# Performance work log

Hardware: AMD Instinct MI355X
Metric: run time of the kernel (lower is better)

The kernel has to match this reference:

```python
import jax, jax.numpy as jnp
import numpy as np

N, L, H, D = 2, 4096, 12, 64
HD = H * D

def setup_inputs() -> dict:
    key = jax.random.key(0)
    ks = jax.random.split(key, 5)
    s = 1.0 / np.sqrt(HD)  # keep projections well-scaled
    return {
        "x": jax.random.normal(ks[0], (N, L, HD), dtype=jnp.float32),
        "Wq": jax.random.normal(ks[1], (HD, HD), dtype=jnp.float32) * s,
        "bq": jnp.zeros((HD,), dtype=jnp.float32),
        "Wk": jax.random.normal(ks[2], (HD, HD), dtype=jnp.float32) * s,
        "bk": jnp.zeros((HD,), dtype=jnp.float32),
        "Wv": jax.random.normal(ks[3], (HD, HD), dtype=jnp.float32) * s,
        "bv": jnp.zeros((HD,), dtype=jnp.float32),
        "Wo": jax.random.normal(ks[4], (HD, HD), dtype=jnp.float32) * s,
        "bo": jnp.zeros((HD,), dtype=jnp.float32),
        "train": 0,
    }

def reference(x, Wq, bq, Wk, bk, Wv, bv, Wo, bo, train):
    n, l, hd = x.shape
    h, d = H, D
    # QKV projections (hk.Linear: x @ W + b), reshape to (n, l, h, d)
    q = (x @ Wq + bq).reshape(n, l, h, d)
    k = (x @ Wk + bk).reshape(n, l, h, d)
    v = (x @ Wv + bv).reshape(n, l, h, d)
    # scores: (n, q, k, h), scaled by sqrt(key_size)
    qkt = jnp.einsum('nqhd,nkhd->nqkh', q, k) / jnp.sqrt(jnp.float32(d))
    attn = jax.nn.softmax(qkt, axis=2)
    # eval mode: dropout_rate is 0.0, so dropout is identity
    o = jnp.einsum('nqkh,nkhd->nqhd', attn, v).reshape(n, l, hd)
    return o @ Wo + bo
```

## Files before the change

### kernel.cpp

```cpp
#include <hip/hip_runtime.h>

#define NN 2
#define LL 4096
#define HH 12
#define DD 64
#define HD_ 768
#define M_TOT (NN * LL)
#define KVSTRIDE 262144

typedef __bf16 bf16_t;
typedef _Float16 f16_t;
typedef __bf16 bf16x8 __attribute__((ext_vector_type(8)));
typedef __bf16 bf16x4 __attribute__((ext_vector_type(4)));
typedef _Float16 f16x2 __attribute__((ext_vector_type(2)));
typedef _Float16 f16x4 __attribute__((ext_vector_type(4)));
typedef _Float16 f16x8 __attribute__((ext_vector_type(8)));
typedef float floatx4 __attribute__((ext_vector_type(4)));
typedef float floatx16 __attribute__((ext_vector_type(16)));

#define QSCALE 0.1803368801111f

__device__ __forceinline__ void async_load16(const void* g, void* l) {
    __builtin_amdgcn_global_load_lds(
        (const __attribute__((address_space(1))) unsigned int*)(g),
        (__attribute__((address_space(3))) unsigned int*)(l),
        16, 0, 0);
}

__device__ __forceinline__ f16x2 pkrtz(float a, float b) {
    return __builtin_bit_cast(f16x2, __builtin_amdgcn_cvt_pkrtz(a, b));
}

__global__ void cvt_kernel(const float* __restrict__ src, bf16_t* __restrict__ dst, int n4) {
    int i = blockIdx.x * blockDim.x + threadIdx.x;
    if (i < n4) {
        const float4 v = ((const float4*)src)[i];
        bf16_t* d = dst + (size_t)i * 4;
        d[0] = (bf16_t)v.x; d[1] = (bf16_t)v.y; d[2] = (bf16_t)v.z; d[3] = (bf16_t)v.w;
    }
}

struct WtArgs { const float* W[4]; bf16_t* Wt[4]; };
__global__ __launch_bounds__(256) void cvt_wt_kernel(WtArgs a) {
    __shared__ bf16_t T[64 * 65];
    const int z = blockIdx.z;
    const int k0 = blockIdx.y * 64, n0 = blockIdx.x * 64;
    const int tid = threadIdx.x;
    {
        const int k = tid >> 2;
        const int nc = (tid & 3) * 16;
        const float* src = a.W[z] + (size_t)(k0 + k) * HD_ + n0 + nc;
        for (int i = 0; i < 4; ++i) {
            float4 v = *(const float4*)(src + i * 4);
            T[(nc + i * 4 + 0) * 65 + k] = (bf16_t)v.x;
            T[(nc + i * 4 + 1) * 65 + k] = (bf16_t)v.y;
            T[(nc + i * 4 + 2) * 65 + k] = (bf16_t)v.z;
            T[(nc + i * 4 + 3) * 65 + k] = (bf16_t)v.w;
        }
    }
    __syncthreads();
    {
        const int n = tid >> 2;
        const int kc = (tid & 3) * 16;
        bf16_t* dst = a.Wt[z] + (size_t)(n0 + n) * HD_ + k0 + kc;
        bf16x8 v0, v1;
        for (int j = 0; j < 8; ++j) { v0[j] = T[n * 65 + kc + j]; v1[j] = T[n * 65 + kc + 8 + j]; }
        *(bf16x8*)dst = v0;
        *(bf16x8*)(dst + 8) = v1;
    }
}

__device__ __forceinline__ void gemm_tile128(
    const bf16_t* __restrict__ A, const bf16_t* __restrict__ Bt,
    bf16_t* As, bf16_t* Bs, int m0, int n0, floatx4 (&acc)[4][4])
{
    const int tid  = threadIdx.x;
    const int w    = tid >> 6, lane = tid & 63;
    const int quad = lane >> 4, l16 = lane & 15;
    const int wm = w >> 1, wn = w & 1;
    const int rsub = lane >> 3;
    const int csub = (lane & 7) * 8;

    const bf16_t* aBase = A + (size_t)(m0 + w * 32 + rsub) * HD_ + csub;
    const bf16_t* bBase = Bt + (size_t)(n0 + w * 32 + rsub) * HD_ + csub;

    for (int kt = 0; kt < HD_; kt += 64) {
        __syncthreads();
        for (int i = 0; i < 4; ++i) {
            const int ar = w * 32 + i * 8;
            async_load16(aBase + (size_t)i * 8 * HD_ + kt, As + ar * 64 + lane * 8);
            async_load16(bBase + (size_t)i * 8 * HD_ + kt, Bs + ar * 64 + lane * 8);
        }
        __syncthreads();
        for (int ks = 0; ks < 2; ++ks) {
            bf16x8 af[4], bf[4];
            for (int mi = 0; mi < 4; ++mi)
                af[mi] = *(const bf16x8*)&As[(wm * 64 + mi * 16 + l16) * 64 + ks * 32 + quad * 8];
            for (int ni = 0; ni < 4; ++ni)
                bf[ni] = *(const bf16x8*)&Bs[(wn * 64 + ni * 16 + l16) * 64 + ks * 32 + quad * 8];
            for (int mi = 0; mi < 4; ++mi)
                for (int ni = 0; ni < 4; ++ni)
                    acc[mi][ni] = __builtin_amdgcn_mfma_f32_16x16x32_bf16(
                        af[mi], bf[ni], acc[mi][ni], 0, 0, 0);
        }
    }
}

struct QKVArgs {
    const bf16_t* Bt[3];
    const float* bias[3];
    void* out[3];
};
__global__ __launch_bounds__(256) void gemm_qkv_kernel(const bf16_t* __restrict__ A, QKVArgs p)
{
    __shared__ __align__(16) bf16_t S[2 * 128 * 64];
    const int z = blockIdx.z;
    const int m0 = blockIdx.y * 128, n0 = blockIdx.x * 128;

    floatx4 acc[4][4] = {};
    gemm_tile128(A, p.Bt[z], S, S + 8192, m0, n0, acc);

    const int tid  = threadIdx.x;
    const int lane = tid & 63;
    const int quad = lane >> 4, l16 = lane & 15;
    const int w    = tid >> 6;
    const int wm = w >> 1, wn = w & 1;
    const float scale = (z == 0) ? QSCALE : 1.0f;
    const float* bias = p.bias[z];

    __syncthreads();
    for (int ni = 0; ni < 4; ++ni) {
        const int dl = ni * 16 + l16;
        const float bv = bias[n0 + wn * 64 + dl];
        for (int mi = 0; mi < 4; ++mi) {
            for (int r = 0; r < 4; ++r) {
                const int ll = wm * 64 + mi * 16 + quad * 4 + r;
                const float val = (acc[mi][ni][r] + bv) * scale;
                int off;
                if (z == 0)
                    off = ll * 64 + dl;
                else if (z == 1)
                    off = ((ll >> 5) * 4 + (dl >> 4)) * 512
                        + ((ll & 31) + 32 * ((dl >> 3) & 1)) * 8 + (dl & 7);
                else
                    off = (((ll >> 6) * 2 + (dl >> 5)) * 4 + ((ll >> 4) & 3)) * 512
                        + ((dl & 31) + 32 * ((ll >> 2) & 1)) * 8
                        + ((ll & 3) + 4 * ((ll >> 3) & 1));
                if (z == 2) ((f16_t*)S)[wn * 8192 + off] = (f16_t)val;
                else        S[wn * 8192 + off] = (bf16_t)val;
            }
        }
    }
    __syncthreads();

    const int ht = tid >> 7, idx = tid & 127;
    const int nn = m0 >> 12, l0 = m0 & 4095;
    const int h = (n0 >> 6) + ht;
    char* dstBase;
    if (z == 0)
        dstBase = (char*)p.out[0] + (((size_t)(nn * HH + h) * LL + l0) * 64) * 2;
    else if (z == 1)
        dstBase = (char*)p.out[1] + ((size_t)(nn * HH + h) * KVSTRIDE + (size_t)(l0 >> 5) * 2048) * 2;
    else
        dstBase = (char*)p.out[2] + ((size_t)(nn * HH + h) * KVSTRIDE + (size_t)(l0 >> 6) * 4096) * 2;
    const bf16_t* srcB = S + ht * 8192;
    for (int c = 0; c < 8; ++c) {
        const int cc = (c + idx) & 7;
        *(bf16x8*)(dstBase + (idx * 64 + cc * 8) * 2) = *(const bf16x8*)(srcB + idx * 64 + cc * 8);
    }
}

__global__ __launch_bounds__(256) void gemm_o_kernel(
    const bf16_t* __restrict__ A, const bf16_t* __restrict__ Bt,
    const float* __restrict__ bias, float* __restrict__ Cout)
{
    __shared__ __align__(16) bf16_t As[128 * 64];
    __shared__ __align__(16) bf16_t Bs[128 * 64];
    const int m0 = blockIdx.y * 128, n0 = blockIdx.x * 128;

    floatx4 acc[4][4] = {};
    gemm_tile128(A, Bt, As, Bs, m0, n0, acc);

    const int tid  = threadIdx.x;
    const int lane = tid & 63;
    const int quad = lane >> 4, l16 = lane & 15;
    const int w    = tid >> 6;
    const int wm = w >> 1, wn = w & 1;

    for (int ni = 0; ni < 4; ++ni) {
        const int col = n0 + wn * 64 + ni * 16 + l16;
        const float bv = bias[col];
        for (int mi = 0; mi < 4; ++mi)
            for (int r = 0; r < 4; ++r) {
                const int row = m0 + wm * 64 + mi * 16 + quad * 4 + r;
                Cout[(size_t)row * HD_ + col] = acc[mi][ni][r] + bv;
            }
    }
}

__global__ __launch_bounds__(256) void attn_kernel(
    const bf16_t* __restrict__ qg, const bf16_t* __restrict__ kf,
    const f16_t* __restrict__ vf, bf16_t* __restrict__ og)
{
    __shared__ union {
        struct { bf16_t Ks[2][8 * 512]; f16_t Vs[2][8 * 512]; } s;
        bf16_t OT[128 * 72];
    } u;

    const int tid = threadIdx.x;
    const int w = tid >> 6, lane = tid & 63;
    const int l32 = lane & 31, hi = lane >> 5;

    const int lb = blockIdx.y * gridDim.x + blockIdx.x;
    const int idx = (lb & 7) * 96 + (lb >> 3);
    const int nh = idx >> 5;
    const int qt0 = (idx & 31) * 128;
    const int nIdx = nh / HH, hIdx = nh % HH;

    bf16x8 qfrag[4];
    {
        const bf16_t* qp = qg + ((size_t)nh * LL + qt0 + w * 32 + l32) * DD + hi * 8;
        for (int s = 0; s < 4; ++s) qfrag[s] = *(const bf16x8*)(qp + s * 16);
    }

    const bf16_t* ksrc = kf + (size_t)nh * KVSTRIDE + (2 * w) * 512 + lane * 8;
    const f16_t*  vsrc = vf + (size_t)nh * KVSTRIDE + (2 * w) * 512 + lane * 8;
    const int soff0 = (2 * w) * 512 + lane * 8;
    const int soff1 = (2 * w + 1) * 512 + lane * 8;

    floatx16 oacc[2] = {};
    float rs = 0.f;

    async_load16(ksrc,       &u.s.Ks[0][soff0]);
    async_load16(ksrc + 512, &u.s.Ks[0][soff1]);
    async_load16(vsrc,       &u.s.Vs[0][soff0]);
    async_load16(vsrc + 512, &u.s.Vs[0][soff1]);
    ksrc += 4096; vsrc += 4096;

    for (int t = 0; t < 64; ++t) {
        const int cur = t & 1;
        __syncthreads();

        if (t < 63) {
            async_load16(ksrc,       &u.s.Ks[cur ^ 1][soff0]);
            async_load16(ksrc + 512, &u.s.Ks[cur ^ 1][soff1]);
            async_load16(vsrc,       &u.s.Vs[cur ^ 1][soff0]);
            async_load16(vsrc + 512, &u.s.Vs[cur ^ 1][soff1]);
            ksrc += 4096; vsrc += 4096;
        }

        for (int kvb = 0; kvb < 2; ++kvb) {
            floatx16 sacc = {};
            for (int s = 0; s < 4; ++s) {
                bf16x8 ak = *(const bf16x8*)&u.s.Ks[cur][(kvb * 4 + s) * 512 + lane * 8];
                sacc = __builtin_amdgcn_mfma_f32_32x32x16_bf16(ak, qfrag[s], sacc, 0, 0, 0);
            }
            for (int sub = 0; sub < 2; ++sub) {
                float p[8];
                for (int i = 0; i < 8; ++i)
                    p[i] = __builtin_amdgcn_exp2f(sacc[sub * 8 + i]);
                rs += ((p[0] + p[1]) + (p[2] + p[3])) + ((p[4] + p[5]) + (p[6] + p[7]));
                f16x2 ab = pkrtz(p[0], p[1]), cd = pkrtz(p[2], p[3]);
                f16x2 ef = pkrtz(p[4], p[5]), gh = pkrtz(p[6], p[7]);
                f16x4 lo4 = __builtin_shufflevector(ab, cd, 0, 1, 2, 3);
                f16x4 hi4 = __builtin_shufflevector(ef, gh, 0, 1, 2, 3);
                f16x8 pf = __builtin_shufflevector(lo4, hi4, 0, 1, 2, 3, 4, 5, 6, 7);
                const int kstep = kvb * 2 + sub;
                for (int db = 0; db < 2; ++db) {
                    f16x8 av = *(const f16x8*)&u.s.Vs[cur][(db * 4 + kstep) * 512 + lane * 8];
                    oacc[db] = __builtin_amdgcn_mfma_f32_32x32x16_f16(av, pf, oacc[db], 0, 0, 0);
                }
            }
        }
    }

    rs += __shfl_xor(rs, 32);
    const float rinv = __builtin_amdgcn_rcpf(rs);

    __syncthreads();
    for (int db = 0; db < 2; ++db)
        for (int g = 0; g < 4; ++g) {
            bf16x4 o4;
            for (int r = 0; r < 4; ++r)
                o4[r] = (bf16_t)(oacc[db][g * 4 + r] * rinv);
            *(bf16x4*)&u.OT[(w * 32 + l32) * 72 + db * 32 + hi * 4 + g * 8] = o4;
        }
    __syncthreads();

    const int q = tid >> 1, hf = tid & 1;
    const bf16_t* src = &u.OT[q * 72 + hf * 32];
    bf16x8 r0 = *(const bf16x8*)(src + 0);
    bf16x8 r1 = *(const bf16x8*)(src + 8);
    bf16x8 r2 = *(const bf16x8*)(src + 16);
    bf16x8 r3 = *(const bf16x8*)(src + 24);
    bf16_t* dst = og + ((size_t)nIdx * LL + qt0 + q) * HD_ + hIdx * 64 + hf * 32;
    *(bf16x8*)(dst + 0)  = r0;
    *(bf16x8*)(dst + 8)  = r1;
    *(bf16x8*)(dst + 16) = r2;
    *(bf16x8*)(dst + 24) = r3;
}

extern "C" void kernel_launch(void* const* d_in, const int* in_sizes, int n_in,
                              void* d_out, int out_size, void* d_ws, size_t ws_size,
                              hipStream_t stream) {
    const float* x  = (const float*)d_in[0];
    const float* Wq = (const float*)d_in[1];
    const float* bq = (const float*)d_in[2];
    const float* Wk = (const float*)d_in[3];
    const float* bk = (const float*)d_in[4];
    const float* Wv = (const float*)d_in[5];
    const float* bv = (const float*)d_in[6];
    const float* Wo = (const float*)d_in[7];
    const float* bo = (const float*)d_in[8];

    char* ws = (char*)d_ws;
    const size_t xbytes = (size_t)M_TOT * HD_ * 2;
    const size_t wbytes = (size_t)HD_ * HD_ * 2;

    bf16_t* xb  = (bf16_t*)ws; ws += xbytes;
    bf16_t* wqt = (bf16_t*)ws; ws += wbytes;
    bf16_t* wkt = (bf16_t*)ws; ws += wbytes;
    bf16_t* wvt = (bf16_t*)ws; ws += wbytes;
    bf16_t* wot = (bf16_t*)ws; ws += wbytes;
    bf16_t* qb  = (bf16_t*)ws; ws += xbytes;
    bf16_t* kfb = (bf16_t*)ws; ws += xbytes;
    f16_t*  vfb = (f16_t*)ws;  ws += xbytes;
    bf16_t* ob  = (bf16_t*)ws; ws += xbytes;

    cvt_kernel<<<(M_TOT * HD_ / 4 + 255) / 256, 256, 0, stream>>>(x, xb, M_TOT * HD_ / 4);

    WtArgs wa;
    wa.W[0] = Wq; wa.W[1] = Wk; wa.W[2] = Wv; wa.W[3] = Wo;
    wa.Wt[0] = wqt; wa.Wt[1] = wkt; wa.Wt[2] = wvt; wa.Wt[3] = wot;
    cvt_wt_kernel<<<dim3(12, 12, 4), 256, 0, stream>>>(wa);

    QKVArgs qa;
    qa.Bt[0] = wqt; qa.Bt[1] = wkt; qa.Bt[2] = wvt;
    qa.bias[0] = bq; qa.bias[1] = bk; qa.bias[2] = bv;
    qa.out[0] = qb; qa.out[1] = kfb; qa.out[2] = vfb;
    gemm_qkv_kernel<<<dim3(HD_ / 128, M_TOT / 128, 3), 256, 0, stream>>>(xb, qa);

    attn_kernel<<<dim3(LL / 128, NN * HH), 256, 0, stream>>>(qb, kfb, vfb, ob);

    gemm_o_kernel<<<dim3(HD_ / 128, M_TOT / 128), 256, 0, stream>>>(ob, wot, bo, (float*)d_out);
}
```

Baseline: 318.6 us.

## Software-pipeline QK^T one tile ahead of PV in attention kernel

```diff
diff --git a/kernel.cpp b/kernel.cpp
--- a/kernel.cpp
+++ b/kernel.cpp
@@ -198,12 +198,15 @@
     }
 }
 
-__global__ __launch_bounds__(256) void attn_kernel(
+__global__ __launch_bounds__(256, 3) void attn_kernel(
     const bf16_t* __restrict__ qg, const bf16_t* __restrict__ kf,
     const f16_t* __restrict__ vf, bf16_t* __restrict__ og)
 {
     __shared__ union {
-        struct { bf16_t Ks[2][8 * 512]; f16_t Vs[2][8 * 512]; } s;
+        struct {
+            bf16_t Ks[2][4096];
+            f16_t  Vs[4][4096];
+        } s;
         bf16_t OT[128 * 72];
     } u;
 
@@ -230,49 +233,77 @@
 
     floatx16 oacc[2] = {};
     float rs = 0.f;
-
-    async_load16(ksrc,       &u.s.Ks[0][soff0]);
-    async_load16(ksrc + 512, &u.s.Ks[0][soff1]);
-    async_load16(vsrc,       &u.s.Vs[0][soff0]);
-    async_load16(vsrc + 512, &u.s.Vs[0][soff1]);
-    ksrc += 4096; vsrc += 4096;
-
-    for (int t = 0; t < 64; ++t) {
-        const int cur = t & 1;
-        __syncthreads();
-
-        if (t < 63) {
-            async_load16(ksrc,       &u.s.Ks[cur ^ 1][soff0]);
-            async_load16(ksrc + 512, &u.s.Ks[cur ^ 1][soff1]);
-            async_load16(vsrc,       &u.s.Vs[cur ^ 1][soff0]);
-            async_load16(vsrc + 512, &u.s.Vs[cur ^ 1][soff1]);
-            ksrc += 4096; vsrc += 4096;
-        }
-
-        for (int kvb = 0; kvb < 2; ++kvb) {
-            floatx16 sacc = {};
-            for (int s = 0; s < 4; ++s) {
-                bf16x8 ak = *(const bf16x8*)&u.s.Ks[cur][(kvb * 4 + s) * 512 + lane * 8];
-                sacc = __builtin_amdgcn_mfma_f32_32x32x16_bf16(ak, qfrag[s], sacc, 0, 0, 0);
-            }
-            for (int sub = 0; sub < 2; ++sub) {
-                float p[8];
-                for (int i = 0; i < 8; ++i)
-                    p[i] = __builtin_amdgcn_exp2f(sacc[sub * 8 + i]);
-                rs += ((p[0] + p[1]) + (p[2] + p[3])) + ((p[4] + p[5]) + (p[6] + p[7]));
-                f16x2 ab = pkrtz(p[0], p[1]), cd = pkrtz(p[2], p[3]);
-                f16x2 ef = pkrtz(p[4], p[5]), gh = pkrtz(p[6], p[7]);
-                f16x4 lo4 = __builtin_shufflevector(ab, cd, 0, 1, 2, 3);
-                f16x4 hi4 = __builtin_shufflevector(ef, gh, 0, 1, 2, 3);
-                f16x8 pf = __builtin_shufflevector(lo4, hi4, 0, 1, 2, 3, 4, 5, 6, 7);
-                const int kstep = kvb * 2 + sub;
-                for (int db = 0; db < 2; ++db) {
-                    f16x8 av = *(const f16x8*)&u.s.Vs[cur][(db * 4 + kstep) * 512 + lane * 8];
-                    oacc[db] = __builtin_amdgcn_mfma_f32_32x32x16_f16(av, pf, oacc[db], 0, 0, 0);
-                }
-            }
-        }
-    }
+    floatx16 sA0, sA1, sB0, sB1;
+
+#define STAGE_K(kb) { async_load16(ksrc, &u.s.Ks[kb][soff0]);                 \
+                      async_load16(ksrc + 512, &u.s.Ks[kb][soff1]);           \
+                      ksrc += 4096; }
+#define STAGE_V(vb) { async_load16(vsrc, &u.s.Vs[vb][soff0]);                 \
+                      async_load16(vsrc + 512, &u.s.Vs[vb][soff1]);           \
+                      vsrc += 4096; }
+
+#define SSTEP(SD0, SD1, kr)                                                   \
+    {                                                                         \
+        SD0 = (floatx16){}; SD1 = (floatx16){};                               \
+        _Pragma("unroll")                                                     \
+        for (int s = 0; s < 4; ++s) {                                         \
+            bf16x8 a0 = *(const bf16x8*)&u.s.Ks[kr][s * 512 + lane * 8];      \
+            SD0 = __builtin_amdgcn_mfma_f32_32x32x16_bf16(a0, qfrag[s], SD0, 0, 0, 0); \
+            bf16x8 a1 = *(const bf16x8*)&u.s.Ks[kr][(4 + s) * 512 + lane * 8]; \
+            SD1 = __builtin_amdgcn_mfma_f32_32x32x16_bf16(a1, qfrag[s], SD1, 0, 0, 0); \
+        }                                                                     \
+    }
+
+#define PHALF(SC, vp, kvb)                                                    \
+    _Pragma("unroll")                                                         \
+    for (int sub = 0; sub < 2; ++sub) {                                       \
+        float p[8];                                                           \
+        _Pragma("unroll")                                                     \
+        for (int i = 0; i < 8; ++i)                                           \
+            p[i] = __builtin_amdgcn_exp2f(SC[sub * 8 + i]);                   \
+        rs += ((p[0] + p[1]) + (p[2] + p[3])) + ((p[4] + p[5]) + (p[6] + p[7])); \
+        f16x2 ab = pkrtz(p[0], p[1]), cd = pkrtz(p[2], p[3]);                 \
+        f16x2 ef = pkrtz(p[4], p[5]), gh = pkrtz(p[6], p[7]);                 \
+        f16x4 lo4 = __builtin_shufflevector(ab, cd, 0, 1, 2, 3);              \
+        f16x4 hi4 = __builtin_shufflevector(ef, gh, 0, 1, 2, 3);              \
+        f16x8 pf = __builtin_shufflevector(lo4, hi4, 0, 1, 2, 3, 4, 5, 6, 7); \
+        const int kstep = (kvb) * 2 + sub;                                    \
+        _Pragma("unroll")                                                     \
+        for (int db = 0; db < 2; ++db) {                                      \
+            f16x8 av = *(const f16x8*)&u.s.Vs[vp][(db * 4 + kstep) * 512 + lane * 8]; \
+            oacc[db] = __builtin_amdgcn_mfma_f32_32x32x16_f16(av, pf, oacc[db], 0, 0, 0); \
+        }                                                                     \
+    }
+
+#define STEP(doDMA, kw, vw, doS, kr, SD0, SD1, SP0, SP1, vp)                  \
+    __syncthreads();                                                          \
+    if (doDMA) { STAGE_K(kw); STAGE_V(vw); }                                  \
+    __builtin_amdgcn_s_setprio(1);                                            \
+    if (doS) SSTEP(SD0, SD1, kr);                                             \
+    PHALF(SP0, vp, 0)                                                         \
+    PHALF(SP1, vp, 1)                                                         \
+    __builtin_amdgcn_s_setprio(0);
+
+    STAGE_K(0) STAGE_V(0) STAGE_K(1) STAGE_V(1)
+    __syncthreads();
+    SSTEP(sA0, sA1, 0);
+
+    for (int t = 0; t < 60; t += 4) {
+        STEP(1, 0, 2, 1, 1, sB0, sB1, sA0, sA1, 0)
+        STEP(1, 1, 3, 1, 0, sA0, sA1, sB0, sB1, 1)
+        STEP(1, 0, 0, 1, 1, sB0, sB1, sA0, sA1, 2)
+        STEP(1, 1, 1, 1, 0, sA0, sA1, sB0, sB1, 3)
+    }
+    STEP(1, 0, 2, 1, 1, sB0, sB1, sA0, sA1, 0)
+    STEP(1, 1, 3, 1, 0, sA0, sA1, sB0, sB1, 1)
+    STEP(0, 0, 0, 1, 1, sB0, sB1, sA0, sA1, 2)
+    STEP(0, 0, 0, 0, 0, sA0, sA1, sB0, sB1, 3)
+
+#undef STEP
+#undef PHALF
+#undef SSTEP
+#undef STAGE_K
+#undef STAGE_V
 
     rs += __shfl_xor(rs, 32);
     const float rinv = __builtin_amdgcn_rcpf(rs);
```

New measurement: 297.8 us. 6.5% less time.

## Have each attention warp process two query sub-tiles to reuse K/V fragments

Applied to the files above, without the earlier changes.

```diff
diff --git a/kernel.cpp b/kernel.cpp
--- a/kernel.cpp
+++ b/kernel.cpp
@@ -29,6 +29,14 @@
 
 __device__ __forceinline__ f16x2 pkrtz(float a, float b) {
     return __builtin_bit_cast(f16x2, __builtin_amdgcn_cvt_pkrtz(a, b));
+}
+
+__device__ __forceinline__ f16x8 pack8(const float* p) {
+    f16x2 ab = pkrtz(p[0], p[1]), cd = pkrtz(p[2], p[3]);
+    f16x2 ef = pkrtz(p[4], p[5]), gh = pkrtz(p[6], p[7]);
+    f16x4 lo4 = __builtin_shufflevector(ab, cd, 0, 1, 2, 3);
+    f16x4 hi4 = __builtin_shufflevector(ef, gh, 0, 1, 2, 3);
+    return __builtin_shufflevector(lo4, hi4, 0, 1, 2, 3, 4, 5, 6, 7);
 }
 
 __global__ void cvt_kernel(const float* __restrict__ src, bf16_t* __restrict__ dst, int n4) {
@@ -198,12 +206,15 @@
     }
 }
 
-__global__ __launch_bounds__(256) void attn_kernel(
+__global__ __launch_bounds__(128, 2) void attn_kernel(
     const bf16_t* __restrict__ qg, const bf16_t* __restrict__ kf,
     const f16_t* __restrict__ vf, bf16_t* __restrict__ og)
 {
     __shared__ union {
-        struct { bf16_t Ks[2][8 * 512]; f16_t Vs[2][8 * 512]; } s;
+        struct {
+            bf16_t Ks[2][4096];
+            f16_t  Vs[2][4096];
+        } s;
         bf16_t OT[128 * 72];
     } u;
 
@@ -217,87 +228,118 @@
     const int qt0 = (idx & 31) * 128;
     const int nIdx = nh / HH, hIdx = nh % HH;
 
-    bf16x8 qfrag[4];
+    bf16x8 qf0[4], qf1[4];
     {
-        const bf16_t* qp = qg + ((size_t)nh * LL + qt0 + w * 32 + l32) * DD + hi * 8;
-        for (int s = 0; s < 4; ++s) qfrag[s] = *(const bf16x8*)(qp + s * 16);
-    }
-
-    const bf16_t* ksrc = kf + (size_t)nh * KVSTRIDE + (2 * w) * 512 + lane * 8;
-    const f16_t*  vsrc = vf + (size_t)nh * KVSTRIDE + (2 * w) * 512 + lane * 8;
-    const int soff0 = (2 * w) * 512 + lane * 8;
-    const int soff1 = (2 * w + 1) * 512 + lane * 8;
-
-    floatx16 oacc[2] = {};
-    float rs = 0.f;
-
-    async_load16(ksrc,       &u.s.Ks[0][soff0]);
-    async_load16(ksrc + 512, &u.s.Ks[0][soff1]);
-    async_load16(vsrc,       &u.s.Vs[0][soff0]);
-    async_load16(vsrc + 512, &u.s.Vs[0][soff1]);
+        const bf16_t* qp0 = qg + ((size_t)nh * LL + qt0 + w * 64 + l32) * DD + hi * 8;
+        const bf16_t* qp1 = qp0 + 32 * DD;
+        #pragma unroll
+        for (int s = 0; s < 4; ++s) {
+            qf0[s] = *(const bf16x8*)(qp0 + s * 16);
+            qf1[s] = *(const bf16x8*)(qp1 + s * 16);
+        }
+    }
+
+    const bf16_t* ksrc = kf + (size_t)nh * KVSTRIDE + tid * 8;
+    const f16_t*  vsrc = vf + (size_t)nh * KVSTRIDE + tid * 8;
+    const int so = tid * 8;
+
+    floatx16 oa0[2] = {}, oa1[2] = {};
+    float rs0 = 0.f, rs1 = 0.f;
+
+    #pragma unroll
+    for (int i = 0; i < 4; ++i) {
+        async_load16(ksrc + i * 1024, &u.s.Ks[0][i * 1024 + so]);
+        async_load16(vsrc + i * 1024, &u.s.Vs[0][i * 1024 + so]);
+    }
     ksrc += 4096; vsrc += 4096;
+
+#define PVSTEP(kstep, SC0, SC1, sub)                                          \
+    {                                                                         \
+        float p0[8], p1[8];                                                   \
+        _Pragma("unroll")                                                     \
+        for (int i = 0; i < 8; ++i) {                                         \
+            p0[i] = __builtin_amdgcn_exp2f(SC0[(sub) * 8 + i]);               \
+            p1[i] = __builtin_amdgcn_exp2f(SC1[(sub) * 8 + i]);               \
+        }                                                                     \
+        rs0 += ((p0[0]+p0[1]) + (p0[2]+p0[3])) + ((p0[4]+p0[5]) + (p0[6]+p0[7])); \
+        rs1 += ((p1[0]+p1[1]) + (p1[2]+p1[3])) + ((p1[4]+p1[5]) + (p1[6]+p1[7])); \
+        f16x8 pf0 = pack8(p0), pf1 = pack8(p1);                               \
+        _Pragma("unroll")                                                     \
+        for (int db = 0; db < 2; ++db) {                                      \
+            f16x8 av = *(const f16x8*)&u.s.Vs[cur][(db * 4 + (kstep)) * 512 + lane * 8]; \
+            oa0[db] = __builtin_amdgcn_mfma_f32_32x32x16_f16(av, pf0, oa0[db], 0, 0, 0); \
+            oa1[db] = __builtin_amdgcn_mfma_f32_32x32x16_f16(av, pf1, oa1[db], 0, 0, 0); \
+        }                                                                     \
+    }
 
     for (int t = 0; t < 64; ++t) {
         const int cur = t & 1;
         __syncthreads();
 
         if (t < 63) {
-            async_load16(ksrc,       &u.s.Ks[cur ^ 1][soff0]);
-            async_load16(ksrc + 512, &u.s.Ks[cur ^ 1][soff1]);
-            async_load16(vsrc,       &u.s.Vs[cur ^ 1][soff0]);
-            async_load16(vsrc + 512, &u.s.Vs[cur ^ 1][soff1]);
+            #pragma unroll
+            for (int i = 0; i < 4; ++i) {
+                async_load16(ksrc + i * 1024, &u.s.Ks[cur ^ 1][i * 1024 + so]);
+                async_load16(vsrc + i * 1024, &u.s.Vs[cur ^ 1][i * 1024 + so]);
+            }
             ksrc += 4096; vsrc += 4096;
         }
 
-        for (int kvb = 0; kvb < 2; ++kvb) {
-            floatx16 sacc = {};
-            for (int s = 0; s < 4; ++s) {
-                bf16x8 ak = *(const bf16x8*)&u.s.Ks[cur][(kvb * 4 + s) * 512 + lane * 8];
-                sacc = __builtin_amdgcn_mfma_f32_32x32x16_bf16(ak, qfrag[s], sacc, 0, 0, 0);
-            }
-            for (int sub = 0; sub < 2; ++sub) {
-                float p[8];
-                for (int i = 0; i < 8; ++i)
-                    p[i] = __builtin_amdgcn_exp2f(sacc[sub * 8 + i]);
-                rs += ((p[0] + p[1]) + (p[2] + p[3])) + ((p[4] + p[5]) + (p[6] + p[7]));
-                f16x2 ab = pkrtz(p[0], p[1]), cd = pkrtz(p[2], p[3]);
-                f16x2 ef = pkrtz(p[4], p[5]), gh = pkrtz(p[6], p[7]);
-                f16x4 lo4 = __builtin_shufflevector(ab, cd, 0, 1, 2, 3);
-                f16x4 hi4 = __builtin_shufflevector(ef, gh, 0, 1, 2, 3);
-                f16x8 pf = __builtin_shufflevector(lo4, hi4, 0, 1, 2, 3, 4, 5, 6, 7);
-                const int kstep = kvb * 2 + sub;
-                for (int db = 0; db < 2; ++db) {
-                    f16x8 av = *(const f16x8*)&u.s.Vs[cur][(db * 4 + kstep) * 512 + lane * 8];
-                    oacc[db] = __builtin_amdgcn_mfma_f32_32x32x16_f16(av, pf, oacc[db], 0, 0, 0);
-                }
-            }
-        }
-    }
-
-    rs += __shfl_xor(rs, 32);
-    const float rinv = __builtin_amdgcn_rcpf(rs);
-
-    __syncthreads();
+        __builtin_amdgcn_s_setprio(1);
+        floatx16 s00 = {}, s01 = {}, s10 = {}, s11 = {};
+        #pragma unroll
+        for (int s = 0; s < 4; ++s) {
+            bf16x8 a0 = *(const bf16x8*)&u.s.Ks[cur][s * 512 + lane * 8];
+            bf16x8 a1 = *(const bf16x8*)&u.s.Ks[cur][(4 + s) * 512 + lane * 8];
+            s00 = __builtin_amdgcn_mfma_f32_32x32x16_bf16(a0, qf0[s], s00, 0, 0, 0);
+            s10 = __builtin_amdgcn_mfma_f32_32x32x16_bf16(a0, qf1[s], s10, 0, 0, 0);
+            s01 = __builtin_amdgcn_mfma_f32_32x32x16_bf16(a1, qf0[s], s01, 0, 0, 0);
+            s11 = __builtin_amdgcn_mfma_f32_32x32x16_bf16(a1, qf1[s], s11, 0, 0, 0);
+        }
+        PVSTEP(0, s00, s10, 0)
+        PVSTEP(1, s00, s10, 1)
+        PVSTEP(2, s01, s11, 0)
+        PVSTEP(3, s01, s11, 1)
+        __builtin_amdgcn_s_setprio(0);
+    }
+#undef PVSTEP
+
+    rs0 += __shfl_xor(rs0, 32);
+    rs1 += __shfl_xor(rs1, 32);
+    const float ri0 = __builtin_amdgcn_rcpf(rs0);
+    const float ri1 = __builtin_amdgcn_rcpf(rs1);
+
+    __syncthreads();
+    #pragma unroll
     for (int db = 0; db < 2; ++db)
-        for (int g = 0; g < 4; ++g) {
+        #pragma unroll
+        for (int g4 = 0; g4 < 4; ++g4) {
             bf16x4 o4;
+            #pragma unroll
             for (int r = 0; r < 4; ++r)
-                o4[r] = (bf16_t)(oacc[db][g * 4 + r] * rinv);
-            *(bf16x4*)&u.OT[(w * 32 + l32) * 72 + db * 32 + hi * 4 + g * 8] = o4;
-        }
-    __syncthreads();
-
-    const int q = tid >> 1, hf = tid & 1;
-    const bf16_t* src = &u.OT[q * 72 + hf * 32];
-    bf16x8 r0 = *(const bf16x8*)(src + 0);
-    bf16x8 r1 = *(const bf16x8*)(src + 8);
-    bf16x8 r2 = *(const bf16x8*)(src + 16);
-    bf16x8 r3 = *(const bf16x8*)(src + 24);
-    bf16_t* dst = og + ((size_t)nIdx * LL + qt0 + q) * HD_ + hIdx * 64 + hf * 32;
-    *(bf16x8*)(dst + 0)  = r0;
-    *(bf16x8*)(dst + 8)  = r1;
-    *(bf16x8*)(dst + 16) = r2;
-    *(bf16x8*)(dst + 24) = r3;
+                o4[r] = (bf16_t)(oa0[db][g4 * 4 + r] * ri0);
+            *(bf16x4*)&u.OT[(w * 64 + l32) * 72 + db * 32 + hi * 4 + g4 * 8] = o4;
+            #pragma unroll
+            for (int r = 0; r < 4; ++r)
+                o4[r] = (bf16_t)(oa1[db][g4 * 4 + r] * ri1);
+            *(bf16x4*)&u.OT[(w * 64 + 32 + l32) * 72 + db * 32 + hi * 4 + g4 * 8] = o4;
+        }
+    __syncthreads();
+
+    #pragma unroll
+    for (int rep = 0; rep < 2; ++rep) {
+        const int q = rep * 64 + (tid >> 1), hf = tid & 1;
+        const bf16_t* src = &u.OT[q * 72 + hf * 32];
+        bf16x8 r0 = *(const bf16x8*)(src + 0);
+        bf16x8 r1 = *(const bf16x8*)(src + 8);
+        bf16x8 r2 = *(const bf16x8*)(src + 16);
+        bf16x8 r3 = *(const bf16x8*)(src + 24);
+        bf16_t* dst = og + ((size_t)nIdx * LL + qt0 + q) * HD_ + hIdx * 64 + hf * 32;
+        *(bf16x8*)(dst + 0)  = r0;
+        *(bf16x8*)(dst + 8)  = r1;
+        *(bf16x8*)(dst + 16) = r2;
+        *(bf16x8*)(dst + 24) = r3;
+    }
 }
 
 extern "C" void kernel_launch(void* const* d_in, const int* in_sizes, int n_in,
@@ -340,7 +382,7 @@
     qa.out[0] = qb; qa.out[1] = kfb; qa.out[2] = vfb;
     gemm_qkv_kernel<<<dim3(HD_ / 128, M_TOT / 128, 3), 256, 0, stream>>>(xb, qa);
 
-    attn_kernel<<<dim3(LL / 128, NN * HH), 256, 0, stream>>>(qb, kfb, vfb, ob);
+    attn_kernel<<<dim3(LL / 128, NN * HH), 128, 0, stream>>>(qb, kfb, vfb, ob);
 
     gemm_o_kernel<<<dim3(HD_ / 128, M_TOT / 128), 256, 0, stream>>>(ob, wot, bo, (float*)d_out);
 }
```

Result: faster. 307.0 us (-3.6%).

## Split attention waves across KV halves with two query tiles each for K/V reuse

Applied to the files above, without the earlier changes.

```diff
diff --git a/kernel.cpp b/kernel.cpp
--- a/kernel.cpp
+++ b/kernel.cpp
@@ -29,6 +29,14 @@
 
 __device__ __forceinline__ f16x2 pkrtz(float a, float b) {
     return __builtin_bit_cast(f16x2, __builtin_amdgcn_cvt_pkrtz(a, b));
+}
+
+__device__ __forceinline__ f16x8 pack8(const float* p) {
+    f16x2 ab = pkrtz(p[0], p[1]), cd = pkrtz(p[2], p[3]);
+    f16x2 ef = pkrtz(p[4], p[5]), gh = pkrtz(p[6], p[7]);
+    f16x4 lo4 = __builtin_shufflevector(ab, cd, 0, 1, 2, 3);
+    f16x4 hi4 = __builtin_shufflevector(ef, gh, 0, 1, 2, 3);
+    return __builtin_shufflevector(lo4, hi4, 0, 1, 2, 3, 4, 5, 6, 7);
 }
 
 __global__ void cvt_kernel(const float* __restrict__ src, bf16_t* __restrict__ dst, int n4) {
@@ -198,18 +206,22 @@
     }
 }
 
-__global__ __launch_bounds__(256) void attn_kernel(
+__global__ __launch_bounds__(256, 3) void attn_kernel(
     const bf16_t* __restrict__ qg, const bf16_t* __restrict__ kf,
     const f16_t* __restrict__ vf, bf16_t* __restrict__ og)
 {
     __shared__ union {
-        struct { bf16_t Ks[2][8 * 512]; f16_t Vs[2][8 * 512]; } s;
-        bf16_t OT[128 * 72];
+        struct { bf16_t Ks[2][4096]; f16_t Vs[2][4096]; } s;
+        struct { float OTF[128][68]; float RS[2][2][2][32]; } e;
     } u;
 
     const int tid = threadIdx.x;
     const int w = tid >> 6, lane = tid & 63;
     const int l32 = lane & 31, hi = lane >> 5;
+    const int qhalf = w >> 1;
+    const int kvh = w & 1;
+    const int kvh4 = kvh * 4;
+    const int kvh2 = kvh * 2;
 
     const int lb = blockIdx.y * gridDim.x + blockIdx.x;
     const int idx = (lb & 7) * 96 + (lb >> 3);
@@ -217,10 +229,15 @@
     const int qt0 = (idx & 31) * 128;
     const int nIdx = nh / HH, hIdx = nh % HH;
 
-    bf16x8 qfrag[4];
+    bf16x8 qf0[4], qf1[4];
     {
-        const bf16_t* qp = qg + ((size_t)nh * LL + qt0 + w * 32 + l32) * DD + hi * 8;
-        for (int s = 0; s < 4; ++s) qfrag[s] = *(const bf16x8*)(qp + s * 16);
+        const bf16_t* qp0 = qg + ((size_t)nh * LL + qt0 + qhalf * 64 + l32) * DD + hi * 8;
+        const bf16_t* qp1 = qp0 + 32 * DD;
+        #pragma unroll
+        for (int s = 0; s < 4; ++s) {
+            qf0[s] = *(const bf16x8*)(qp0 + s * 16);
+            qf1[s] = *(const bf16x8*)(qp1 + s * 16);
+        }
     }
 
     const bf16_t* ksrc = kf + (size_t)nh * KVSTRIDE + (2 * w) * 512 + lane * 8;
@@ -228,8 +245,8 @@
     const int soff0 = (2 * w) * 512 + lane * 8;
     const int soff1 = (2 * w + 1) * 512 + lane * 8;
 
-    floatx16 oacc[2] = {};
-    float rs = 0.f;
+    floatx16 oa0[2] = {}, oa1[2] = {};
+    float rs0 = 0.f, rs1 = 0.f;
 
     async_load16(ksrc,       &u.s.Ks[0][soff0]);
     async_load16(ksrc + 512, &u.s.Ks[0][soff1]);
@@ -249,55 +266,96 @@
             ksrc += 4096; vsrc += 4096;
         }
 
-        for (int kvb = 0; kvb < 2; ++kvb) {
-            floatx16 sacc = {};
-            for (int s = 0; s < 4; ++s) {
-                bf16x8 ak = *(const bf16x8*)&u.s.Ks[cur][(kvb * 4 + s) * 512 + lane * 8];
-                sacc = __builtin_amdgcn_mfma_f32_32x32x16_bf16(ak, qfrag[s], sacc, 0, 0, 0);
-            }
-            for (int sub = 0; sub < 2; ++sub) {
-                float p[8];
-                for (int i = 0; i < 8; ++i)
-                    p[i] = __builtin_amdgcn_exp2f(sacc[sub * 8 + i]);
-                rs += ((p[0] + p[1]) + (p[2] + p[3])) + ((p[4] + p[5]) + (p[6] + p[7]));
-                f16x2 ab = pkrtz(p[0], p[1]), cd = pkrtz(p[2], p[3]);
-                f16x2 ef = pkrtz(p[4], p[5]), gh = pkrtz(p[6], p[7]);
-                f16x4 lo4 = __builtin_shufflevector(ab, cd, 0, 1, 2, 3);
-                f16x4 hi4 = __builtin_shufflevector(ef, gh, 0, 1, 2, 3);
-                f16x8 pf = __builtin_shufflevector(lo4, hi4, 0, 1, 2, 3, 4, 5, 6, 7);
-                const int kstep = kvb * 2 + sub;
-                for (int db = 0; db < 2; ++db) {
-                    f16x8 av = *(const f16x8*)&u.s.Vs[cur][(db * 4 + kstep) * 512 + lane * 8];
-                    oacc[db] = __builtin_amdgcn_mfma_f32_32x32x16_f16(av, pf, oacc[db], 0, 0, 0);
+        __builtin_amdgcn_s_setprio(1);
+        floatx16 s0 = {}, s1 = {};
+        #pragma unroll
+        for (int s = 0; s < 4; ++s) {
+            bf16x8 ak = *(const bf16x8*)&u.s.Ks[cur][(kvh4 + s) * 512 + lane * 8];
+            s0 = __builtin_amdgcn_mfma_f32_32x32x16_bf16(ak, qf0[s], s0, 0, 0, 0);
+            s1 = __builtin_amdgcn_mfma_f32_32x32x16_bf16(ak, qf1[s], s1, 0, 0, 0);
+        }
+        #pragma unroll
+        for (int sub = 0; sub < 2; ++sub) {
+            float p0[8], p1[8];
+            #pragma unroll
+            for (int i = 0; i < 8; ++i) {
+                p0[i] = __builtin_amdgcn_exp2f(s0[sub * 8 + i]);
+                p1[i] = __builtin_amdgcn_exp2f(s1[sub * 8 + i]);
+            }
+            rs0 += ((p0[0]+p0[1]) + (p0[2]+p0[3])) + ((p0[4]+p0[5]) + (p0[6]+p0[7]));
+            rs1 += ((p1[0]+p1[1]) + (p1[2]+p1[3])) + ((p1[4]+p1[5]) + (p1[6]+p1[7]));
+            f16x8 pf0 = pack8(p0), pf1 = pack8(p1);
+            #pragma unroll
+            for (int db = 0; db < 2; ++db) {
+                f16x8 av = *(const f16x8*)&u.s.Vs[cur][(db * 4 + kvh2 + sub) * 512 + lane * 8];
+                oa0[db] = __builtin_amdgcn_mfma_f32_32x32x16_f16(av, pf0, oa0[db], 0, 0, 0);
+                oa1[db] = __builtin_amdgcn_mfma_f32_32x32x16_f16(av, pf1, oa1[db], 0, 0, 0);
+            }
+        }
+        __builtin_amdgcn_s_setprio(0);
+    }
+
+    rs0 += __shfl_xor(rs0, 32);
+    rs1 += __shfl_xor(rs1, 32);
+
+    __syncthreads();
+    if (hi == 0) {
+        u.e.RS[qhalf][0][kvh][l32] = rs0;
+        u.e.RS[qhalf][1][kvh][l32] = rs1;
+    }
+    __syncthreads();
+    const float ri0 = __builtin_amdgcn_rcpf(u.e.RS[qhalf][0][0][l32] + u.e.RS[qhalf][0][1][l32]);
+    const float ri1 = __builtin_amdgcn_rcpf(u.e.RS[qhalf][1][0][l32] + u.e.RS[qhalf][1][1][l32]);
+
+    const int q0 = qhalf * 64 + l32, q1 = q0 + 32;
+    if (kvh == 0) {
+        #pragma unroll
+        for (int db = 0; db < 2; ++db)
+            #pragma unroll
+            for (int g4 = 0; g4 < 4; ++g4) {
+                const int d0 = db * 32 + hi * 4 + g4 * 8;
+                floatx4 v0, v1;
+                #pragma unroll
+                for (int r = 0; r < 4; ++r) {
+                    v0[r] = oa0[db][g4 * 4 + r];
+                    v1[r] = oa1[db][g4 * 4 + r];
                 }
-            }
-        }
-    }
-
-    rs += __shfl_xor(rs, 32);
-    const float rinv = __builtin_amdgcn_rcpf(rs);
-
-    __syncthreads();
-    for (int db = 0; db < 2; ++db)
-        for (int g = 0; g < 4; ++g) {
-            bf16x4 o4;
-            for (int r = 0; r < 4; ++r)
-                o4[r] = (bf16_t)(oacc[db][g * 4 + r] * rinv);
-            *(bf16x4*)&u.OT[(w * 32 + l32) * 72 + db * 32 + hi * 4 + g * 8] = o4;
-        }
+                *(floatx4*)&u.e.OTF[q0][d0] = v0;
+                *(floatx4*)&u.e.OTF[q1][d0] = v1;
+            }
+    }
+    __syncthreads();
+    if (kvh == 1) {
+        #pragma unroll
+        for (int db = 0; db < 2; ++db)
+            #pragma unroll
+            for (int g4 = 0; g4 < 4; ++g4) {
+                const int d0 = db * 32 + hi * 4 + g4 * 8;
+                floatx4 v0 = *(const floatx4*)&u.e.OTF[q0][d0];
+                floatx4 v1 = *(const floatx4*)&u.e.OTF[q1][d0];
+                #pragma unroll
+                for (int r = 0; r < 4; ++r) {
+                    v0[r] = (v0[r] + oa0[db][g4 * 4 + r]) * ri0;
+                    v1[r] = (v1[r] + oa1[db][g4 * 4 + r]) * ri1;
+                }
+                *(floatx4*)&u.e.OTF[q0][d0] = v0;
+                *(floatx4*)&u.e.OTF[q1][d0] = v1;
+            }
+    }
     __syncthreads();
 
     const int q = tid >> 1, hf = tid & 1;
-    const bf16_t* src = &u.OT[q * 72 + hf * 32];
-    bf16x8 r0 = *(const bf16x8*)(src + 0);
-    bf16x8 r1 = *(const bf16x8*)(src + 8);
-    bf16x8 r2 = *(const bf16x8*)(src + 16);
-    bf16x8 r3 = *(const bf16x8*)(src + 24);
+    const float* srcf = &u.e.OTF[q][hf * 32];
+    bf16x8 outv[4];
+    #pragma unroll
+    for (int b = 0; b < 4; ++b)
+        #pragma unroll
+        for (int j = 0; j < 8; ++j)
+            outv[b][j] = (bf16_t)srcf[b * 8 + j];
     bf16_t* dst = og + ((size_t)nIdx * LL + qt0 + q) * HD_ + hIdx * 64 + hf * 32;
-    *(bf16x8*)(dst + 0)  = r0;
-    *(bf16x8*)(dst + 8)  = r1;
-    *(bf16x8*)(dst + 16) = r2;
-    *(bf16x8*)(dst + 24) = r3;
+    #pragma unroll
+    for (int b = 0; b < 4; ++b)
+        *(bf16x8*)(dst + b * 8) = outv[b];
 }
 
 extern "C" void kernel_launch(void* const* d_in, const int* in_sizes, int n_in,
```

Measured after the change: 312.5 us. About the same (-1.9%).
